# Performance work log

Hardware: AMD Instinct MI355X
Metric: run time of the kernel (lower is better)

Reference implementation:

```python
import jax, jax.numpy as jnp
import numpy as np

HEADS = 8
HDIM = 64
MAX_PEMB = 512


def setup_inputs() -> dict:
    key = jax.random.key(0)
    ks = jax.random.split(key, 6)
    B, S, D = 4, 1024, 512
    return {
        "x": jax.random.normal(ks[0], (B, S, D), jnp.float32),
        "attn_mask": jnp.ones((B, S), jnp.bool_),
        "Wq": jax.random.normal(ks[1], (D, HEADS * HDIM), jnp.float32) * 0.02,
        "Wkv": jax.random.normal(ks[2], (D, 2 * HEADS * HDIM), jnp.float32) * 0.02,
        "Wout": jax.random.normal(ks[3], (HEADS * HDIM, D), jnp.float32) * 0.02,
        "bout": jnp.zeros((D,), jnp.float32),
        "pemb": jax.random.normal(ks[4], (2 * MAX_PEMB + 1, HDIM), jnp.float32) * 0.02,
    }


def reference(x, attn_mask, Wq, Wkv, Wout, bout, pemb):
    # attn_mask is unpacked but unused in the original call(); faithful to source.
    B, S, D = x.shape
    scale = HDIM ** (-0.5)

    q = (x @ Wq).reshape(B, S, HEADS, HDIM).transpose(0, 2, 1, 3)  # [B,H,S,hd]
    kv = x @ Wkv
    k, v = jnp.split(kv, 2, axis=-1)
    k = k.reshape(B, S, HEADS, HDIM).transpose(0, 2, 1, 3)
    v = v.reshape(B, S, HEADS, HDIM).transpose(0, 2, 1, 3)

    attn_score = jnp.einsum('bhqd,bhkd->bhqk', q, k) * scale

    seq = jnp.arange(S)
    dist = jnp.clip(seq[:, None] - seq[None, :], -MAX_PEMB, MAX_PEMB) + MAX_PEMB  # [S,S]
    rel_pemb = pemb[dist]  # [S,S,hd]
    pos_attn = jnp.einsum('bhsd,std->bhst', q, rel_pemb) * scale  # [B,H,S,S]

    attn_probs = jax.nn.softmax(attn_score + pos_attn, axis=-1)
    ctx = jnp.einsum('bhqk,bhkd->bqhd', attn_probs, v).reshape(B, S, HEADS * HDIM)
    return ctx @ Wout + bout
```

## Files before the change

### kernel.cpp

```cpp
#include <hip/hip_runtime.h>
#include <hip/hip_bf16.h>

constexpr int BATCH = 4;
constexpr int SEQ   = 1024;
constexpr int DM    = 512;
constexpr int NH    = 8;
constexpr int HD    = 64;
constexpr int NQKV  = 1536;

typedef unsigned short u16;
typedef __attribute__((ext_vector_type(8))) __bf16 bf8;
typedef __attribute__((ext_vector_type(4))) __bf16 bf4;
typedef __attribute__((ext_vector_type(4))) float  f4;
typedef __attribute__((ext_vector_type(16))) float f16v;

#define MFMA16(a, b, c) __builtin_amdgcn_mfma_f32_16x16x32_bf16(a, b, c, 0, 0, 0)
#define MFMA32(a, b, c) __builtin_amdgcn_mfma_f32_32x32x16_bf16(a, b, c, 0, 0, 0)

#define QSC 0.18033688f

static __device__ __forceinline__ u16 f2b(float f) {
    union { float f; unsigned u; } v; v.f = f;
    unsigned r = v.u + 0x7FFFu + ((v.u >> 16) & 1u);
    return (u16)(r >> 16);
}
static __device__ __forceinline__ float fexp2(float x) {
    return __builtin_amdgcn_exp2f(x);
}
static __device__ __forceinline__ void gl_lds16(const void* g, void* l) {
    __builtin_amdgcn_global_load_lds(
        (const __attribute__((address_space(1))) void*)g,
        (__attribute__((address_space(3))) void*)l, 16, 0, 0);
}
static __device__ __forceinline__ unsigned cvtpk_bf16(float lo, float hi) {
    unsigned r;
    asm("v_cvt_pk_bf16_f32 %0, %1, %2" : "=v"(r) : "v"(lo), "v"(hi));
    return r;
}
static __device__ __forceinline__ void swap32(unsigned &a, unsigned &b) {
    asm("v_permlane32_swap_b32 %0, %1" : "+v"(a), "+v"(b));
}

__device__ __forceinline__ void tcvt_tile(const float* __restrict__ in,
                                          u16* __restrict__ out,
                                          int R, int C, int bx, int by, int tid,
                                          float (*t)[33]) {
    int r0 = by * 32, c0 = bx * 32;
    int lc = tid & 31, lr = tid >> 5;
    #pragma unroll
    for (int p = 0; p < 4; p++) {
        int r = lr + p * 8;
        t[r][lc] = in[(size_t)(r0 + r) * C + c0 + lc];
    }
    __syncthreads();
    #pragma unroll
    for (int p = 0; p < 4; p++) {
        int r = lr + p * 8;
        out[(size_t)(c0 + r) * R + r0 + lc] = f2b(t[lc][r]);
    }
}

__global__ __launch_bounds__(256)
void prep(const float* __restrict__ x, const float* __restrict__ Wq,
          const float* __restrict__ Wkv, const float* __restrict__ Wout,
          const float* __restrict__ pemb,
          u16* __restrict__ xb, u16* __restrict__ qkvw,
          u16* __restrict__ Woutt, u16* __restrict__ pembb) {
    __shared__ float t[32][33];
    const int blk = blockIdx.x, tid = threadIdx.x;
    if (blk < 2048) {
        int i = (blk * 256 + tid) * 4;
        float4 v = *(const float4*)(x + i);
        ushort4 o = {f2b(v.x), f2b(v.y), f2b(v.z), f2b(v.w)};
        *(ushort4*)(xb + i) = o;
    } else if (blk < 2113) {
        int i = ((blk - 2048) * 256 + tid) * 4;
        if (i < 1025 * HD) {
            float4 v = *(const float4*)(pemb + i);
            ushort4 o = {f2b(v.x), f2b(v.y), f2b(v.z), f2b(v.w)};
            *(ushort4*)(pembb + i) = o;
        }
    } else if (blk < 2369) {
        int l = blk - 2113;
        tcvt_tile(Wq, qkvw, 512, 512, l & 15, l >> 4, tid, t);
    } else if (blk < 2881) {
        int l = blk - 2369;
        tcvt_tile(Wkv, qkvw + 512 * 512, 512, 1024, l & 31, l >> 5, tid, t);
    } else {
        int l = blk - 2881;
        tcvt_tile(Wout, Woutt, 512, 512, l & 15, l >> 4, tid, t);
    }
}

__global__ __launch_bounds__(256)
void gemm_bt(const u16* __restrict__ A, const u16* __restrict__ Bt,
             int M, int N, int K,
             float* __restrict__ Cf, const float* __restrict__ bias,
             __bf16* __restrict__ qtb, __bf16* __restrict__ ktb,
             __bf16* __restrict__ vtb) {
    __shared__ __align__(16) u16 As[2][64][32];
    __shared__ __align__(16) u16 Bs[2][128][32];
    const int tid = threadIdx.x, w = tid >> 6, lane = tid & 63;
    const int l15 = lane & 15, l4 = lane >> 4;
    const int wr = (w >> 1) * 32, wc = (w & 1) * 64;
    const int bm = blockIdx.y * 64, bn = blockIdx.x * 128;

    f4 acc[2][4];
    #pragma unroll
    for (int i = 0; i < 2; i++)
        #pragma unroll
        for (int j = 0; j < 4; j++) acc[i][j] = (f4){0.f, 0.f, 0.f, 0.f};

    const int rS = lane >> 2;
    const int cS = (lane & 3) * 8;

    for (int k0 = 0; k0 < K; k0 += 64) {
        #pragma unroll
        for (int ks = 0; ks < 2; ks++) {
            gl_lds16(A + (size_t)(bm + w * 16 + rS) * K + k0 + ks * 32 + cS,
                     &As[ks][w * 16][0]);
            gl_lds16(Bt + (size_t)(bn + w * 32 + rS) * K + k0 + ks * 32 + cS,
                     &Bs[ks][w * 32][0]);
            gl_lds16(Bt + (size_t)(bn + w * 32 + 16 + rS) * K + k0 + ks * 32 + cS,
                     &Bs[ks][w * 32 + 16][0]);
        }
        __syncthreads();
        #pragma unroll
        for (int ks = 0; ks < 2; ks++) {
            bf8 af[2], bf[4];
            #pragma unroll
            for (int i = 0; i < 2; i++)
                af[i] = *(const bf8*)&As[ks][wr + i * 16 + l15][l4 * 8];
            #pragma unroll
            for (int j = 0; j < 4; j++)
                bf[j] = *(const bf8*)&Bs[ks][wc + j * 16 + l15][l4 * 8];
            #pragma unroll
            for (int i = 0; i < 2; i++)
                #pragma unroll
                for (int j = 0; j < 4; j++)
                    acc[i][j] = MFMA16(af[i], bf[j], acc[i][j]);
        }
        __syncthreads();
    }
    #pragma unroll
    for (int i = 0; i < 2; i++)
        #pragma unroll
        for (int j = 0; j < 4; j++) {
            const int col = bn + wc + j * 16 + l15;
            const int row0 = bm + wr + i * 16 + l4 * 4;
            if (Cf) {
                #pragma unroll
                for (int reg = 0; reg < 4; reg++)
                    Cf[(size_t)(row0 + reg) * N + col] = acc[i][j][reg] + bias[col];
            } else if (col < 512) {
                int h = col >> 6, d = col & 63;
                #pragma unroll
                for (int reg = 0; reg < 4; reg++) {
                    int row = row0 + reg;
                    int b = row >> 10, t = row & 1023;
                    qtb[((((size_t)(b * 8 + h)) << 10 | t) << 6) | d] =
                        (__bf16)(acc[i][j][reg] * QSC);
                }
            } else if (col < 1024) {
                int h = (col >> 6) - 8, d = col & 63;
                #pragma unroll
                for (int reg = 0; reg < 4; reg++) {
                    int row = row0 + reg;
                    int b = row >> 10, t = row & 1023;
                    ktb[((((size_t)(b * 8 + h)) << 10 | t) << 6) | d] =
                        (__bf16)acc[i][j][reg];
                }
            } else {
                int h = (col >> 6) - 16, d = col & 63;
                int b = row0 >> 10, t = row0 & 1023;
                __bf16 pk[4];
                #pragma unroll
                for (int reg = 0; reg < 4; reg++) pk[reg] = (__bf16)acc[i][j][reg];
                *(ushort4*)&vtb[(((size_t)(b * 8 + h) * 64 + d) << 10) | t] =
                    *(ushort4*)pk;
            }
        }
}

__global__ __launch_bounds__(256)
void attn_mfma(const u16* __restrict__ qtb, const u16* __restrict__ ktb,
               const u16* __restrict__ vtb, const u16* __restrict__ pembb,
               __bf16* __restrict__ ctxb) {
    __shared__ __align__(16) __bf16 Kb[2][64][72];
    __shared__ __align__(16) __bf16 Vb[2][64][72];
    __shared__ __align__(16) __bf16 Qd[256][72];

    const int tid = threadIdx.x, w = tid >> 6, lane = tid & 63;
    const int l31 = lane & 31, hi = lane >> 5;
    const int wq = w >> 1, wt = w & 1;
    const int bh = blockIdx.x, b = bh >> 3;
    const int s0 = blockIdx.y * 64;

    bf8 qb[4];
    {
        const u16* qp = qtb + ((size_t)bh * SEQ + s0 + wq * 32 + l31) * HD + hi * 8;
        #pragma unroll
        for (int st = 0; st < 4; st++) qb[st] = *(const bf8*)(qp + st * 16);
    }

    #pragma unroll
    for (int pass = 0; pass < 2; pass++) {
        const int jr = s0 + 449 + pass * 64 + wt * 32 + l31;
        const int jc = min(1024, max(0, jr));
        const u16* pp = pembb + (size_t)jc * HD + hi * 8;
        f16v acc;
        #pragma unroll
        for (int r = 0; r < 16; r++) acc[r] = 0.f;
        #pragma unroll
        for (int st = 0; st < 4; st++) {
            bf8 pj = *(const bf8*)(pp + st * 16);
            acc = MFMA32(qb[st], pj, acc);
        }
        #pragma unroll
        for (int o4 = 0; o4 < 4; o4++) {
            bf4 pk;
            #pragma unroll
            for (int r = 0; r < 4; r++) pk[r] = (__bf16)acc[o4 * 4 + r];
            *(bf4*)&Qd[jr & 255][wq * 32 + o4 * 8 + hi * 4] = pk;
        }
    }

    float l_lane = 0.f;
    f16v oo[2];
    #pragma unroll
    for (int dt = 0; dt < 2; dt++)
        #pragma unroll
        for (int r = 0; r < 16; r++) oo[dt][r] = 0.f;

    const u16* kbase = ktb + (size_t)bh * SEQ * HD;
    const u16* vbase = vtb + (size_t)bh * HD * SEQ;
    const int sr = tid >> 3, sc = (tid & 7) * 8;

    *(bf8*)&Kb[0][sr][sc]      = *(const bf8*)(kbase + (size_t)sr * HD + sc);
    *(bf8*)&Kb[0][sr + 32][sc] = *(const bf8*)(kbase + (size_t)(sr + 32) * HD + sc);
    *(bf8*)&Vb[0][sr][sc]      = *(const bf8*)(vbase + (size_t)sr * SEQ + sc);
    *(bf8*)&Vb[0][sr + 32][sc] = *(const bf8*)(vbase + (size_t)(sr + 32) * SEQ + sc);
    __syncthreads();

    for (int i = 0; i < 16; i++) {
        const int cur = i & 1, nxt = cur ^ 1;
        const int t0 = i * 64, t1 = t0 + 64;
        const bool pre = (i < 15);
        bf8 kr0, kr1, vr0, vr1, pj0, pj1, pj2, pj3;
        const int jrn = s0 + 449 - 64 * (i + 1) + wt * 32 + l31;
        if (pre) {
            kr0 = *(const bf8*)(kbase + (size_t)(t1 + sr) * HD + sc);
            kr1 = *(const bf8*)(kbase + (size_t)(t1 + sr + 32) * HD + sc);
            vr0 = *(const bf8*)(vbase + (size_t)sr * SEQ + t1 + sc);
            vr1 = *(const bf8*)(vbase + (size_t)(sr + 32) * SEQ + t1 + sc);
            const int jc = min(1024, max(0, jrn));
            const u16* pp = pembb + (size_t)jc * HD + hi * 8;
            pj0 = *(const bf8*)(pp);
            pj1 = *(const bf8*)(pp + 16);
            pj2 = *(const bf8*)(pp + 32);
            pj3 = *(const bf8*)(pp + 48);
        }

        f16v s16;
        #pragma unroll
        for (int r = 0; r < 16; r++) s16[r] = 0.f;
        #pragma unroll
        for (int st = 0; st < 4; st++) {
            bf8 ka = *(const bf8*)&Kb[cur][wt * 32 + l31][st * 16 + hi * 8];
            s16 = MFMA32(ka, qb[st], s16);
        }
        bf8 vf00 = *(const bf8*)&Vb[cur][l31][wt * 32 + hi * 8];
        bf8 vf01 = *(const bf8*)&Vb[cur][l31][wt * 32 + 16 + hi * 8];
        bf8 vf10 = *(const bf8*)&Vb[cur][32 + l31][wt * 32 + hi * 8];
        bf8 vf11 = *(const bf8*)&Vb[cur][32 + l31][wt * 32 + 16 + hi * 8];

        const int jcst = (s0 - t0 + 512) + wq * 32 + l31 - wt * 32 - 4 * hi;
        const __bf16* qdc = &Qd[0][wq * 32 + l31];
        float p[16];
        #pragma unroll
        for (int r = 0; r < 16; r++) {
            const int pat = (r & 3) + 8 * (r >> 2);
            const int j = (jcst - pat) & 255;
            float pv = fexp2(s16[r] + (float)qdc[j * 72]);
            p[r] = pv;
            l_lane += pv;
        }
        unsigned w00 = cvtpk_bf16(p[0],  p[1]),  w01 = cvtpk_bf16(p[2],  p[3]);
        unsigned w10 = cvtpk_bf16(p[4],  p[5]),  w11 = cvtpk_bf16(p[6],  p[7]);
        unsigned w20 = cvtpk_bf16(p[8],  p[9]),  w21 = cvtpk_bf16(p[10], p[11]);
        unsigned w30 = cvtpk_bf16(p[12], p[13]), w31 = cvtpk_bf16(p[14], p[15]);
        swap32(w00, w10); swap32(w01, w11);
        swap32(w20, w30); swap32(w21, w31);
        union { unsigned u[4]; bf8 v; } pa0, pa1;
        pa0.u[0] = w00; pa0.u[1] = w01; pa0.u[2] = w10; pa0.u[3] = w11;
        pa1.u[0] = w20; pa1.u[1] = w21; pa1.u[2] = w30; pa1.u[3] = w31;
        oo[0] = MFMA32(pa0.v, vf00, oo[0]);
        oo[0] = MFMA32(pa1.v, vf01, oo[0]);
        oo[1] = MFMA32(pa0.v, vf10, oo[1]);
        oo[1] = MFMA32(pa1.v, vf11, oo[1]);

        if (pre) {
            f16v rf;
            #pragma unroll
            for (int r = 0; r < 16; r++) rf[r] = 0.f;
            rf = MFMA32(qb[0], pj0, rf);
            rf = MFMA32(qb[1], pj1, rf);
            rf = MFMA32(qb[2], pj2, rf);
            rf = MFMA32(qb[3], pj3, rf);
            #pragma unroll
            for (int o4 = 0; o4 < 4; o4++) {
                bf4 pk;
                #pragma unroll
                for (int r = 0; r < 4; r++) pk[r] = (__bf16)rf[o4 * 4 + r];
                *(bf4*)&Qd[jrn & 255][wq * 32 + o4 * 8 + hi * 4] = pk;
            }
            *(bf8*)&Kb[nxt][sr][sc]      = kr0;
            *(bf8*)&Kb[nxt][sr + 32][sc] = kr1;
            *(bf8*)&Vb[nxt][sr][sc]      = vr0;
            *(bf8*)&Vb[nxt][sr + 32][sc] = vr1;
        }
        __syncthreads();
    }

    float lsum = l_lane + __shfl_xor(l_lane, 32);
    float* Os = (float*)&Qd[0][0];
    float* Ls = Os + 4096;
    if (lane < 32) Ls[(wq * 2 + wt) * 32 + l31] = lsum;
    if (wt == 0) {
        #pragma unroll
        for (int dt = 0; dt < 2; dt++)
            #pragma unroll
            for (int r = 0; r < 16; r++) {
                const int q = (r & 3) + 8 * (r >> 2) + 4 * hi;
                Os[(wq * 32 + q) * 64 + dt * 32 + l31] = oo[dt][r];
            }
    }
    __syncthreads();
    if (wt == 1) {
        const int h = bh & 7;
        #pragma unroll
        for (int r = 0; r < 16; r++) {
            const int q = (r & 3) + 8 * (r >> 2) + 4 * hi;
            const float li = 1.f / (Ls[wq * 64 + q] + Ls[wq * 64 + 32 + q]);
            #pragma unroll
            for (int dt = 0; dt < 2; dt++) {
                float v = (oo[dt][r] + Os[(wq * 32 + q) * 64 + dt * 32 + l31]) * li;
                ctxb[(size_t)(b * SEQ + s0 + wq * 32 + q) * DM + h * HD + dt * 32 + l31]
                    = (__bf16)v;
            }
        }
    }
}

extern "C" void kernel_launch(void* const* d_in, const int* in_sizes, int n_in,
                              void* d_out, int out_size, void* d_ws, size_t ws_size,
                              hipStream_t stream) {
    const float* x    = (const float*)d_in[0];
    const float* Wq   = (const float*)d_in[2];
    const float* Wkv  = (const float*)d_in[3];
    const float* Wout = (const float*)d_in[4];
    const float* bout = (const float*)d_in[5];
    const float* pemb = (const float*)d_in[6];
    float* out = (float*)d_out;

    const int M = BATCH * SEQ;
    u16* p = (u16*)d_ws;
    u16* xb    = p; p += (size_t)M * DM;
    u16* qkvw  = p; p += (size_t)NQKV * DM;
    u16* Woutt = p; p += (size_t)DM * DM;
    u16* pembb = p; p += (size_t)1025 * HD;
    u16* qtb   = p; p += (size_t)M * DM;
    u16* ktb   = p; p += (size_t)M * DM;
    u16* vtb   = p; p += (size_t)M * DM;
    u16* ctxb  = p; p += (size_t)M * DM;

    prep<<<3137, 256, 0, stream>>>(x, Wq, Wkv, Wout, pemb, xb, qkvw, Woutt, pembb);

    gemm_bt<<<dim3(NQKV / 128, M / 64), 256, 0, stream>>>(
        xb, qkvw, M, NQKV, DM, nullptr, nullptr,
        (__bf16*)qtb, (__bf16*)ktb, (__bf16*)vtb);

    attn_mfma<<<dim3(BATCH * NH, SEQ / 64), 256, 0, stream>>>(
        qtb, ktb, vtb, pembb, (__bf16*)ctxb);

    gemm_bt<<<dim3(DM / 128, M / 64), 256, 0, stream>>>(
        ctxb, Woutt, M, DM, DM, out, bout, nullptr, nullptr, nullptr);
}
```

Baseline: 127.3 us.

## Interleave softmax exp with PV MFMAs in attention; narrow output GEMM tile

The attention inner loop now issues all K fragment and rel-position LDS reads before the QK MFMAs. It then splits the exp/convert/PV work into two halves so the first half's PV MFMAs can run while the second half's exponentials are computed, and raises wave priority with s_setprio around that region. The GEMM kernel is templated on its N tile width, and the output projection uses a 64-wide tile, doubling its block count to improve occupancy on the small N=512 GEMM. Trade-offs are higher register pressure from holding more fragments and smaller per-block reuse in the output GEMM.

```diff
diff --git a/kernel.cpp b/kernel.cpp
--- a/kernel.cpp
+++ b/kernel.cpp
@@ -23,6 +23,10 @@
     union { float f; unsigned u; } v; v.f = f;
     unsigned r = v.u + 0x7FFFu + ((v.u >> 16) & 1u);
     return (u16)(r >> 16);
+}
+static __device__ __forceinline__ float b2f(u16 x) {
+    union { unsigned u; float f; } v; v.u = (unsigned)x << 16;
+    return v.f;
 }
 static __device__ __forceinline__ float fexp2(float x) {
     return __builtin_amdgcn_exp2f(x);
@@ -92,24 +96,26 @@
     }
 }
 
+template<int BN>
 __global__ __launch_bounds__(256)
 void gemm_bt(const u16* __restrict__ A, const u16* __restrict__ Bt,
              int M, int N, int K,
              float* __restrict__ Cf, const float* __restrict__ bias,
              __bf16* __restrict__ qtb, __bf16* __restrict__ ktb,
              __bf16* __restrict__ vtb) {
+    constexpr int NJ = BN / 32;
     __shared__ __align__(16) u16 As[2][64][32];
-    __shared__ __align__(16) u16 Bs[2][128][32];
+    __shared__ __align__(16) u16 Bs[2][BN][32];
     const int tid = threadIdx.x, w = tid >> 6, lane = tid & 63;
     const int l15 = lane & 15, l4 = lane >> 4;
-    const int wr = (w >> 1) * 32, wc = (w & 1) * 64;
-    const int bm = blockIdx.y * 64, bn = blockIdx.x * 128;
-
-    f4 acc[2][4];
+    const int wr = (w >> 1) * 32, wc = (w & 1) * (BN / 2);
+    const int bm = blockIdx.y * 64, bn = blockIdx.x * BN;
+
+    f4 acc[2][NJ];
     #pragma unroll
     for (int i = 0; i < 2; i++)
         #pragma unroll
-        for (int j = 0; j < 4; j++) acc[i][j] = (f4){0.f, 0.f, 0.f, 0.f};
+        for (int j = 0; j < NJ; j++) acc[i][j] = (f4){0.f, 0.f, 0.f, 0.f};
 
     const int rS = lane >> 2;
     const int cS = (lane & 3) * 8;
@@ -119,25 +125,26 @@
         for (int ks = 0; ks < 2; ks++) {
             gl_lds16(A + (size_t)(bm + w * 16 + rS) * K + k0 + ks * 32 + cS,
                      &As[ks][w * 16][0]);
-            gl_lds16(Bt + (size_t)(bn + w * 32 + rS) * K + k0 + ks * 32 + cS,
-                     &Bs[ks][w * 32][0]);
-            gl_lds16(Bt + (size_t)(bn + w * 32 + 16 + rS) * K + k0 + ks * 32 + cS,
-                     &Bs[ks][w * 32 + 16][0]);
+            #pragma unroll
+            for (int rb = 0; rb < BN / 4; rb += 16)
+                gl_lds16(Bt + (size_t)(bn + w * (BN / 4) + rb + rS) * K
+                             + k0 + ks * 32 + cS,
+                         &Bs[ks][w * (BN / 4) + rb][0]);
         }
         __syncthreads();
         #pragma unroll
         for (int ks = 0; ks < 2; ks++) {
-            bf8 af[2], bf[4];
+            bf8 af[2], bf[NJ];
             #pragma unroll
             for (int i = 0; i < 2; i++)
                 af[i] = *(const bf8*)&As[ks][wr + i * 16 + l15][l4 * 8];
             #pragma unroll
-            for (int j = 0; j < 4; j++)
+            for (int j = 0; j < NJ; j++)
                 bf[j] = *(const bf8*)&Bs[ks][wc + j * 16 + l15][l4 * 8];
             #pragma unroll
             for (int i = 0; i < 2; i++)
                 #pragma unroll
-                for (int j = 0; j < 4; j++)
+                for (int j = 0; j < NJ; j++)
                     acc[i][j] = MFMA16(af[i], bf[j], acc[i][j]);
         }
         __syncthreads();
@@ -145,7 +152,7 @@
     #pragma unroll
     for (int i = 0; i < 2; i++)
         #pragma unroll
-        for (int j = 0; j < 4; j++) {
+        for (int j = 0; j < NJ; j++) {
             const int col = bn + wc + j * 16 + l15;
             const int row0 = bm + wr + i * 16 + l4 * 4;
             if (Cf) {
@@ -261,43 +268,57 @@
             pj3 = *(const bf8*)(pp + 48);
         }
 
-        f16v s16;
-        #pragma unroll
-        for (int r = 0; r < 16; r++) s16[r] = 0.f;
-        #pragma unroll
-        for (int st = 0; st < 4; st++) {
-            bf8 ka = *(const bf8*)&Kb[cur][wt * 32 + l31][st * 16 + hi * 8];
-            s16 = MFMA32(ka, qb[st], s16);
+        bf8 ka[4];
+        #pragma unroll
+        for (int st = 0; st < 4; st++)
+            ka[st] = *(const bf8*)&Kb[cur][wt * 32 + l31][st * 16 + hi * 8];
+        const int jcst = (s0 - t0 + 512) + wq * 32 + l31 - wt * 32 - 4 * hi;
+        const u16* qdc = (const u16*)&Qd[0][0] + wq * 32 + l31;
+        u16 rg[16];
+        #pragma unroll
+        for (int r = 0; r < 16; r++) {
+            const int pat = (r & 3) + 8 * (r >> 2);
+            rg[r] = qdc[((jcst - pat) & 255) * 72];
         }
         bf8 vf00 = *(const bf8*)&Vb[cur][l31][wt * 32 + hi * 8];
         bf8 vf01 = *(const bf8*)&Vb[cur][l31][wt * 32 + 16 + hi * 8];
         bf8 vf10 = *(const bf8*)&Vb[cur][32 + l31][wt * 32 + hi * 8];
         bf8 vf11 = *(const bf8*)&Vb[cur][32 + l31][wt * 32 + 16 + hi * 8];
 
-        const int jcst = (s0 - t0 + 512) + wq * 32 + l31 - wt * 32 - 4 * hi;
-        const __bf16* qdc = &Qd[0][wq * 32 + l31];
+        __builtin_amdgcn_s_setprio(1);
+        f16v s16;
+        #pragma unroll
+        for (int r = 0; r < 16; r++) s16[r] = 0.f;
+        #pragma unroll
+        for (int st = 0; st < 4; st++) s16 = MFMA32(ka[st], qb[st], s16);
+
         float p[16];
-        #pragma unroll
-        for (int r = 0; r < 16; r++) {
-            const int pat = (r & 3) + 8 * (r >> 2);
-            const int j = (jcst - pat) & 255;
-            float pv = fexp2(s16[r] + (float)qdc[j * 72]);
-            p[r] = pv;
-            l_lane += pv;
-        }
-        unsigned w00 = cvtpk_bf16(p[0],  p[1]),  w01 = cvtpk_bf16(p[2],  p[3]);
-        unsigned w10 = cvtpk_bf16(p[4],  p[5]),  w11 = cvtpk_bf16(p[6],  p[7]);
+        float la = 0.f, lb = 0.f;
+        #pragma unroll
+        for (int r = 0; r < 8; r++) {
+            float pv = fexp2(s16[r] + b2f(rg[r]));
+            p[r] = pv; la += pv;
+        }
+        unsigned w00 = cvtpk_bf16(p[0], p[1]), w01 = cvtpk_bf16(p[2], p[3]);
+        unsigned w10 = cvtpk_bf16(p[4], p[5]), w11 = cvtpk_bf16(p[6], p[7]);
+        swap32(w00, w10); swap32(w01, w11);
+        union { unsigned u[4]; bf8 v; } pa0, pa1;
+        pa0.u[0] = w00; pa0.u[1] = w01; pa0.u[2] = w10; pa0.u[3] = w11;
+        oo[0] = MFMA32(pa0.v, vf00, oo[0]);
+        oo[1] = MFMA32(pa0.v, vf10, oo[1]);
+        #pragma unroll
+        for (int r = 8; r < 16; r++) {
+            float pv = fexp2(s16[r] + b2f(rg[r]));
+            p[r] = pv; lb += pv;
+        }
         unsigned w20 = cvtpk_bf16(p[8],  p[9]),  w21 = cvtpk_bf16(p[10], p[11]);
         unsigned w30 = cvtpk_bf16(p[12], p[13]), w31 = cvtpk_bf16(p[14], p[15]);
-        swap32(w00, w10); swap32(w01, w11);
         swap32(w20, w30); swap32(w21, w31);
-        union { unsigned u[4]; bf8 v; } pa0, pa1;
-        pa0.u[0] = w00; pa0.u[1] = w01; pa0.u[2] = w10; pa0.u[3] = w11;
         pa1.u[0] = w20; pa1.u[1] = w21; pa1.u[2] = w30; pa1.u[3] = w31;
-        oo[0] = MFMA32(pa0.v, vf00, oo[0]);
         oo[0] = MFMA32(pa1.v, vf01, oo[0]);
-        oo[1] = MFMA32(pa0.v, vf10, oo[1]);
         oo[1] = MFMA32(pa1.v, vf11, oo[1]);
+        __builtin_amdgcn_s_setprio(0);
+        l_lane += la + lb;
 
         if (pre) {
             f16v rf;
@@ -376,13 +397,13 @@
 
     prep<<<3137, 256, 0, stream>>>(x, Wq, Wkv, Wout, pemb, xb, qkvw, Woutt, pembb);
 
-    gemm_bt<<<dim3(NQKV / 128, M / 64), 256, 0, stream>>>(
+    gemm_bt<128><<<dim3(NQKV / 128, M / 64), 256, 0, stream>>>(
         xb, qkvw, M, NQKV, DM, nullptr, nullptr,
         (__bf16*)qtb, (__bf16*)ktb, (__bf16*)vtb);
 
     attn_mfma<<<dim3(BATCH * NH, SEQ / 64), 256, 0, stream>>>(
         qtb, ktb, vtb, pembb, (__bf16*)ctxb);
 
-    gemm_bt<<<dim3(DM / 128, M / 64), 256, 0, stream>>>(
+    gemm_bt<64><<<dim3(DM / 64, M / 64), 256, 0, stream>>>(
         ctxb, Woutt, M, DM, DM, out, bout, nullptr, nullptr, nullptr);
 }
```

Measured after the change: 124.6 us. 1.02x faster.
